# Kernel tuning notes

Hardware: AMD Instinct MI355X
Metric: run time of the kernel (lower is better)

The kernel has to match this reference:

```python
import jax, jax.numpy as jnp
import numpy as np

ALPHA_MAX = 0.1


def setup_inputs() -> dict:
    key = jax.random.key(0)
    ks = jax.random.split(key, 9)
    B, M, L = 256, 3, 100000
    A, H = 4096, 512
    return {
        "x": jax.random.uniform(ks[0], (B, M, L), dtype=jnp.float32),  # log1p scores, non-negative
        "active_idx": jax.random.randint(ks[1], (A,), 0, L, dtype=jnp.int64 if jax.config.jax_enable_x64 else jnp.int32),
        "global_logits": jnp.log(jnp.full((M,), 1.0 / M, dtype=jnp.float32) + 1e-12),
        "delta_w": 0.01 * jax.random.normal(ks[2], (M, L), dtype=jnp.float32),
        "bias": 0.01 * jax.random.normal(ks[3], (L,), dtype=jnp.float32),
        "log_alpha": jnp.float32(-3.0),
        "hidden_w": jax.random.normal(ks[4], (H, M * A), dtype=jnp.float32) * (1.0 / np.sqrt(M * A)),
        "hidden_b": 0.01 * jax.random.normal(ks[5], (H,), dtype=jnp.float32),
        "delta_layer_w": jax.random.normal(ks[6], (A, H), dtype=jnp.float32) * (1.0 / np.sqrt(H)),
        "delta_layer_b": 0.01 * jax.random.normal(ks[7], (A,), dtype=jnp.float32),
    }


def reference(x, active_idx, global_logits, delta_w, bias, log_alpha,
              hidden_w, hidden_b, delta_layer_w, delta_layer_b):
    B = x.shape[0]
    # base logits: elementwise weighted sum over the 3 models, per-label weights
    w_eff = jax.nn.softmax(global_logits)[:, None] + delta_w          # (M, L)
    logits = jnp.einsum("bml,ml->bl", x, w_eff) + bias                # (B, L)
    # gather active labels -> 2-layer MLP (dropout is identity in eval)
    x_active = x[:, :, active_idx].reshape(B, -1)                     # (B, M*A)
    h = jax.nn.relu(x_active @ hidden_w.T + hidden_b)                 # (B, H)
    delta_active = h @ delta_layer_w.T + delta_layer_b                # (B, A)
    # scaled scatter-add back into full logits (duplicates accumulate)
    alpha = ALPHA_MAX * jax.nn.sigmoid(log_alpha)
    logits = logits.at[:, active_idx].add(alpha * delta_active)
    return logits
```

## Files before the change

kernel.cpp:

```cpp
#include <hip/hip_runtime.h>
#include <math.h>

#define B_ 256
#define M_ 3
#define L_ 100000
#define A_ 4096
#define H_ 512
#define MA_ (M_*A_)
#define K1_ MA_
#define NZ_ 16
#define KC1_ (K1_/NZ_)
#define BCHUNK_ 4

#define NB_LG_   6272
#define NB_LGX_  98
#define NB_HW_   3072
#define NB_W2_   1024

typedef __attribute__((ext_vector_type(8))) short bf16x8;
typedef __attribute__((ext_vector_type(8))) unsigned short u16x8;
typedef __attribute__((ext_vector_type(4))) float f32x4;
typedef __attribute__((ext_vector_type(4))) int i32x4;

static __device__ __forceinline__ f32x4 ld4(const float* p) {
    return *reinterpret_cast<const f32x4*>(p);
}
static __device__ __forceinline__ f32x4 ld4nt(const float* p) {
    return __builtin_nontemporal_load(reinterpret_cast<const f32x4*>(p));
}
static __device__ __forceinline__ void st4nt(float* p, f32x4 v) {
    __builtin_nontemporal_store(v, reinterpret_cast<f32x4*>(p));
}
static __device__ __forceinline__ unsigned short f2bf(float f) {
    unsigned u = __float_as_uint(f);
    unsigned r = (u + 0x7FFFu + ((u >> 16) & 1u)) >> 16;
    return (unsigned short)r;
}

__global__ void init_head(int* __restrict__ head) {
    int i = blockIdx.x * blockDim.x + threadIdx.x;
    if (i < L_ / 4) {
        i32x4 m1 = {-1, -1, -1, -1};
        *reinterpret_cast<i32x4*>(head + i * 4) = m1;
    }
}

__global__ void build_head(const int* __restrict__ idx, int* __restrict__ head) {
    int a = blockIdx.x * blockDim.x + threadIdx.x;
    if (a < A_) head[idx[a]] = a;
}

__global__ __launch_bounds__(256) void mega(
    const float* __restrict__ x, const float* __restrict__ gl,
    const float* __restrict__ dw, const float* __restrict__ bias,
    const int* __restrict__ head,
    float* __restrict__ logits, unsigned short* __restrict__ xa,
    const float* __restrict__ hw, unsigned short* __restrict__ hwb,
    const float* __restrict__ w2, unsigned short* __restrict__ w2b) {
    int bid = blockIdx.x;
    int tid = threadIdx.x;

    if (bid >= NB_LG_) {
        const float* src;
        unsigned short* dst;
        int i;
        if (bid < NB_LG_ + NB_HW_) { src = hw; dst = hwb; i = (bid - NB_LG_) * 256 + tid; }
        else                       { src = w2; dst = w2b; i = (bid - NB_LG_ - NB_HW_) * 256 + tid; }
        f32x4 v0 = ld4nt(src + (size_t)i * 8);
        f32x4 v1 = ld4nt(src + (size_t)i * 8 + 4);
        u16x8 o;
        o[0] = f2bf(v0.x); o[1] = f2bf(v0.y); o[2] = f2bf(v0.z); o[3] = f2bf(v0.w);
        o[4] = f2bf(v1.x); o[5] = f2bf(v1.y); o[6] = f2bf(v1.z); o[7] = f2bf(v1.w);
        *reinterpret_cast<u16x8*>(dst + (size_t)i * 8) = o;
        return;
    }

    const int L4 = L_ / 4;
    int i = (bid % NB_LGX_) * 256 + tid;
    if (i >= L4) return;
    int l = i * 4;
    int b0 = (bid / NB_LGX_) * BCHUNK_;

    float g0 = gl[0], g1 = gl[1], g2 = gl[2];
    float mx = fmaxf(g0, fmaxf(g1, g2));
    float e0 = expf(g0 - mx), e1 = expf(g1 - mx), e2 = expf(g2 - mx);
    float inv = 1.0f / (e0 + e1 + e2);
    float s0 = e0 * inv, s1 = e1 * inv, s2 = e2 * inv;

    f32x4 d0 = ld4(dw + l);
    f32x4 d1 = ld4(dw + L_ + l);
    f32x4 d2 = ld4(dw + 2 * L_ + l);
    f32x4 bb = ld4(bias + l);
    f32x4 w0 = d0 + s0;
    f32x4 w1 = d1 + s1;
    f32x4 w2v = d2 + s2;

    i32x4 heads = *reinterpret_cast<const i32x4*>(head + l);

    f32x4 X[BCHUNK_][3];
    #pragma unroll
    for (int c = 0; c < BCHUNK_; ++c) {
        const float* xb = x + (size_t)(b0 + c) * M_ * L_ + l;
        X[c][0] = ld4nt(xb);
        X[c][1] = ld4nt(xb + L_);
        X[c][2] = ld4nt(xb + 2 * L_);
    }
    #pragma unroll
    for (int c = 0; c < BCHUNK_; ++c) {
        f32x4 o = X[c][0] * w0 + X[c][1] * w1 + X[c][2] * w2v + bb;
        st4nt(logits + (size_t)(b0 + c) * L_ + l, o);
    }

    #pragma unroll
    for (int c = 0; c < 4; ++c) {
        int a = heads[c];
        if (a >= 0) {
            #pragma unroll
            for (int b = 0; b < BCHUNK_; ++b) {
                unsigned short* xab = xa + (size_t)(b0 + b) * MA_;
                xab[a]          = f2bf(X[b][0][c]);
                xab[A_ + a]     = f2bf(X[b][1][c]);
                xab[2 * A_ + a] = f2bf(X[b][2][c]);
            }
        }
    }
}

__global__ void fixup(const int* __restrict__ idx, const int* __restrict__ head,
                      unsigned short* __restrict__ xa) {
    int t = blockIdx.x * blockDim.x + threadIdx.x;
    if (t >= B_ * A_) return;
    int a = t & (A_ - 1);
    int b = t >> 12;
    int ha = head[idx[a]];
    if (ha == a) return;
    unsigned short* xab = xa + (size_t)b * MA_;
    xab[a]          = xab[ha];
    xab[A_ + a]     = xab[A_ + ha];
    xab[2 * A_ + a] = xab[2 * A_ + ha];
}

__global__ __launch_bounds__(256) void gemm1_mfma(
    const unsigned short* __restrict__ Xa, const unsigned short* __restrict__ W,
    float* __restrict__ part) {
    int tid = threadIdx.x;
    int wave = tid >> 6, lane = tid & 63;
    int row0 = blockIdx.x * 64 + (wave >> 1) * 32;
    int col0 = blockIdx.y * 64 + (wave & 1) * 32;
    int k0 = blockIdx.z * KC1_;
    int lr = lane & 15;
    int lk = (lane >> 4) * 8;
    const unsigned short* pa0 = Xa + (size_t)(row0 + lr) * K1_ + k0 + lk;
    const unsigned short* pa1 = pa0 + (size_t)16 * K1_;
    const unsigned short* pb0 = W + (size_t)(col0 + lr) * K1_ + k0 + lk;
    const unsigned short* pb1 = pb0 + (size_t)16 * K1_;
    f32x4 acc00 = {0.f,0.f,0.f,0.f}, acc01 = {0.f,0.f,0.f,0.f};
    f32x4 acc10 = {0.f,0.f,0.f,0.f}, acc11 = {0.f,0.f,0.f,0.f};
    #pragma unroll 4
    for (int k = 0; k < KC1_; k += 32) {
        bf16x8 a0 = *reinterpret_cast<const bf16x8*>(pa0 + k);
        bf16x8 a1 = *reinterpret_cast<const bf16x8*>(pa1 + k);
        bf16x8 b0 = *reinterpret_cast<const bf16x8*>(pb0 + k);
        bf16x8 b1 = *reinterpret_cast<const bf16x8*>(pb1 + k);
        acc00 = __builtin_amdgcn_mfma_f32_16x16x32_bf16(a0, b0, acc00, 0, 0, 0);
        acc01 = __builtin_amdgcn_mfma_f32_16x16x32_bf16(a0, b1, acc01, 0, 0, 0);
        acc10 = __builtin_amdgcn_mfma_f32_16x16x32_bf16(a1, b0, acc10, 0, 0, 0);
        acc11 = __builtin_amdgcn_mfma_f32_16x16x32_bf16(a1, b1, acc11, 0, 0, 0);
    }
    float* base = part + (size_t)blockIdx.z * B_ * H_;
    #pragma unroll
    for (int j = 0; j < 4; ++j) {
        int r = (lane >> 4) * 4 + j;
        base[(size_t)(row0 + r) * H_ + col0 + lr]           = acc00[j];
        base[(size_t)(row0 + r) * H_ + col0 + 16 + lr]      = acc01[j];
        base[(size_t)(row0 + 16 + r) * H_ + col0 + lr]      = acc10[j];
        base[(size_t)(row0 + 16 + r) * H_ + col0 + 16 + lr] = acc11[j];
    }
}

__global__ void reduce_relu(const float* __restrict__ part,
                            const float* __restrict__ hb,
                            unsigned short* __restrict__ h) {
    int t = blockIdx.x * blockDim.x + threadIdx.x;
    if (t >= B_ * H_) return;
    int n = t & (H_ - 1);
    float s = hb[n];
    #pragma unroll
    for (int z = 0; z < NZ_; ++z) s += part[(size_t)z * B_ * H_ + t];
    h[t] = f2bf(fmaxf(s, 0.0f));
}

__global__ __launch_bounds__(256) void gemm2_scatter(
    const unsigned short* __restrict__ Hm, const unsigned short* __restrict__ W2,
    const float* __restrict__ b2, const float* __restrict__ la,
    const int* __restrict__ idx, float* __restrict__ logits) {
    int tid = threadIdx.x;
    int wave = tid >> 6, lane = tid & 63;
    int row0 = blockIdx.x * 64 + (wave >> 1) * 32;
    int col0 = blockIdx.y * 64 + (wave & 1) * 32;
    int lr = lane & 15;
    int lk = (lane >> 4) * 8;
    const unsigned short* pa0 = Hm + (size_t)(row0 + lr) * H_ + lk;
    const unsigned short* pa1 = pa0 + (size_t)16 * H_;
    const unsigned short* pb0 = W2 + (size_t)(col0 + lr) * H_ + lk;
    const unsigned short* pb1 = pb0 + (size_t)16 * H_;
    f32x4 acc00 = {0.f,0.f,0.f,0.f}, acc01 = {0.f,0.f,0.f,0.f};
    f32x4 acc10 = {0.f,0.f,0.f,0.f}, acc11 = {0.f,0.f,0.f,0.f};
    #pragma unroll 4
    for (int k = 0; k < H_; k += 32) {
        bf16x8 a0 = *reinterpret_cast<const bf16x8*>(pa0 + k);
        bf16x8 a1 = *reinterpret_cast<const bf16x8*>(pa1 + k);
        bf16x8 b0 = *reinterpret_cast<const bf16x8*>(pb0 + k);
        bf16x8 b1 = *reinterpret_cast<const bf16x8*>(pb1 + k);
        acc00 = __builtin_amdgcn_mfma_f32_16x16x32_bf16(a0, b0, acc00, 0, 0, 0);
        acc01 = __builtin_amdgcn_mfma_f32_16x16x32_bf16(a0, b1, acc01, 0, 0, 0);
        acc10 = __builtin_amdgcn_mfma_f32_16x16x32_bf16(a1, b0, acc10, 0, 0, 0);
        acc11 = __builtin_amdgcn_mfma_f32_16x16x32_bf16(a1, b1, acc11, 0, 0, 0);
    }
    float alpha = 0.1f / (1.0f + expf(-la[0]));
    int c0 = col0 + lr, c1 = col0 + 16 + lr;
    int l0 = idx[c0], l1 = idx[c1];
    float bias0 = b2[c0], bias1 = b2[c1];
    #pragma unroll
    for (int j = 0; j < 4; ++j) {
        int r = (lane >> 4) * 4 + j;
        atomicAdd(&logits[(size_t)(row0 + r) * L_ + l0],      alpha * (acc00[j] + bias0));
        atomicAdd(&logits[(size_t)(row0 + r) * L_ + l1],      alpha * (acc01[j] + bias1));
        atomicAdd(&logits[(size_t)(row0 + 16 + r) * L_ + l0], alpha * (acc10[j] + bias0));
        atomicAdd(&logits[(size_t)(row0 + 16 + r) * L_ + l1], alpha * (acc11[j] + bias1));
    }
}

static inline size_t align256(size_t x) { return (x + 255) & ~(size_t)255; }

extern "C" void kernel_launch(void* const* d_in, const int* in_sizes, int n_in,
                              void* d_out, int out_size, void* d_ws, size_t ws_size,
                              hipStream_t stream) {
    const float* x    = (const float*)d_in[0];
    const int*   idx  = (const int*)d_in[1];
    const float* gl   = (const float*)d_in[2];
    const float* dw   = (const float*)d_in[3];
    const float* bias = (const float*)d_in[4];
    const float* la   = (const float*)d_in[5];
    const float* hw   = (const float*)d_in[6];
    const float* hb   = (const float*)d_in[7];
    const float* w2   = (const float*)d_in[8];
    const float* b2   = (const float*)d_in[9];
    float* logits = (float*)d_out;

    char* ws = (char*)d_ws;
    int* head = (int*)ws;                      ws += align256((size_t)L_ * 4);
    unsigned short* xa = (unsigned short*)ws;  ws += align256((size_t)B_ * MA_ * 2);
    unsigned short* hwb = (unsigned short*)ws; ws += align256((size_t)H_ * MA_ * 2);
    unsigned short* w2b = (unsigned short*)ws; ws += align256((size_t)A_ * H_ * 2);
    float* part = (float*)ws;                  ws += align256((size_t)NZ_ * B_ * H_ * 4);
    unsigned short* h = (unsigned short*)ws;   ws += align256((size_t)B_ * H_ * 2);

    init_head<<<(L_ / 4 + 255) / 256, 256, 0, stream>>>(head);
    build_head<<<(A_ + 255) / 256, 256, 0, stream>>>(idx, head);

    mega<<<NB_LG_ + NB_HW_ + NB_W2_, 256, 0, stream>>>(
        x, gl, dw, bias, head, logits, xa, hw, hwb, w2, w2b);

    fixup<<<(B_ * A_ + 255) / 256, 256, 0, stream>>>(idx, head, xa);

    gemm1_mfma<<<dim3(B_ / 64, H_ / 64, NZ_), 256, 0, stream>>>(xa, hwb, part);
    reduce_relu<<<(B_ * H_ + 255) / 256, 256, 0, stream>>>(part, hb, h);
    gemm2_scatter<<<dim3(B_ / 64, A_ / 64), 256, 0, stream>>>(h, w2b, b2, la, idx, logits);
}
```

Baseline: 202.3 us.

## Sort active labels into positional order so xa writes are local; drop fixup pass

Builds a permutation of the active indices sorted by label position, using a per-window histogram and rank-based placement. The gathered activation matrix xa is then written in sorted column order, and duplicate labels are written directly, so the separate fixup kernel is removed. The K dimension of the hidden weight is permuted to match while it is cast to bf16. The point is to make the scattered xa writes contiguous per window and save one launch, at the cost of two small setup kernels and gathered reads of hidden_w during the conversion.

```diff
diff --git a/kernel.cpp b/kernel.cpp
--- a/kernel.cpp
+++ b/kernel.cpp
@@ -12,8 +12,9 @@
 #define KC1_ (K1_/NZ_)
 #define BCHUNK_ 4
 
-#define NB_LG_   6272
+#define NWIN_    98
 #define NB_LGX_  98
+#define NB_LG_   (NB_LGX_*(B_/BCHUNK_))
 #define NB_HW_   3072
 #define NB_W2_   1024
 
@@ -45,15 +46,56 @@
     }
 }
 
-__global__ void build_head(const int* __restrict__ idx, int* __restrict__ head) {
-    int a = blockIdx.x * blockDim.x + threadIdx.x;
-    if (a < A_) head[idx[a]] = a;
+__global__ void window_hist(const int* __restrict__ idx, int* __restrict__ jbase) {
+    __shared__ int cnt[NWIN_];
+    for (int w = threadIdx.x; w < NWIN_; w += 256) cnt[w] = 0;
+    __syncthreads();
+    for (int a = threadIdx.x; a < A_; a += 256) atomicAdd(&cnt[idx[a] >> 10], 1);
+    __syncthreads();
+    if (threadIdx.x == 0) {
+        int s = 0;
+        for (int w = 0; w < NWIN_; ++w) { jbase[w] = s; s += cnt[w]; }
+        jbase[NWIN_] = s;
+    }
+}
+
+__global__ void build_perm(const int* __restrict__ idx, const int* __restrict__ jbase,
+                           int* __restrict__ a_of_j, int* __restrict__ l_of_j,
+                           int* __restrict__ head2) {
+    __shared__ int ml[A_];
+    __shared__ int ma[A_];
+    __shared__ int nm_sh;
+    int w = blockIdx.x, tid = threadIdx.x;
+    if (tid == 0) nm_sh = 0;
+    __syncthreads();
+    for (int a = tid; a < A_; a += 256) {
+        int l = idx[a];
+        if ((l >> 10) == w) { int p = atomicAdd(&nm_sh, 1); ml[p] = l; ma[p] = a; }
+    }
+    __syncthreads();
+    int nm = nm_sh;
+    int base = jbase[w];
+    for (int p = tid; p < nm; p += 256) {
+        int l = ml[p], a = ma[p];
+        int rank = 0, same_smaller = 0;
+        for (int q = 0; q < nm; ++q) {
+            int lq = ml[q], aq = ma[q];
+            rank += (lq < l) | ((lq == l) & (aq < a));
+            same_smaller += ((lq == l) & (aq < a));
+        }
+        int j = base + rank;
+        a_of_j[j] = a;
+        l_of_j[j] = l;
+        if (same_smaller == 0) head2[l] = j;
+    }
+    if (w == 0 && tid == 0) l_of_j[A_] = -1;
 }
 
 __global__ __launch_bounds__(256) void mega(
     const float* __restrict__ x, const float* __restrict__ gl,
     const float* __restrict__ dw, const float* __restrict__ bias,
-    const int* __restrict__ head,
+    const int* __restrict__ head2, const int* __restrict__ l_of_j,
+    const int* __restrict__ a_of_j,
     float* __restrict__ logits, unsigned short* __restrict__ xa,
     const float* __restrict__ hw, unsigned short* __restrict__ hwb,
     const float* __restrict__ w2, unsigned short* __restrict__ w2b) {
@@ -61,17 +103,26 @@
     int tid = threadIdx.x;
 
     if (bid >= NB_LG_) {
-        const float* src;
-        unsigned short* dst;
-        int i;
-        if (bid < NB_LG_ + NB_HW_) { src = hw; dst = hwb; i = (bid - NB_LG_) * 256 + tid; }
-        else                       { src = w2; dst = w2b; i = (bid - NB_LG_ - NB_HW_) * 256 + tid; }
-        f32x4 v0 = ld4nt(src + (size_t)i * 8);
-        f32x4 v1 = ld4nt(src + (size_t)i * 8 + 4);
-        u16x8 o;
-        o[0] = f2bf(v0.x); o[1] = f2bf(v0.y); o[2] = f2bf(v0.z); o[3] = f2bf(v0.w);
-        o[4] = f2bf(v1.x); o[5] = f2bf(v1.y); o[6] = f2bf(v1.z); o[7] = f2bf(v1.w);
-        *reinterpret_cast<u16x8*>(dst + (size_t)i * 8) = o;
+        if (bid < NB_LG_ + NB_HW_) {
+            int i = (bid - NB_LG_) * 256 + tid;
+            int o = i * 8;
+            int n = o / MA_;
+            int col = o % MA_;
+            int m = col >> 12, j0 = col & (A_ - 1);
+            const float* row = hw + (size_t)n * MA_ + (m << 12);
+            u16x8 out;
+            #pragma unroll
+            for (int t = 0; t < 8; ++t) out[t] = f2bf(row[a_of_j[j0 + t]]);
+            *reinterpret_cast<u16x8*>(hwb + (size_t)o) = out;
+        } else {
+            int i = (bid - NB_LG_ - NB_HW_) * 256 + tid;
+            f32x4 v0 = ld4nt(w2 + (size_t)i * 8);
+            f32x4 v1 = ld4nt(w2 + (size_t)i * 8 + 4);
+            u16x8 o;
+            o[0] = f2bf(v0.x); o[1] = f2bf(v0.y); o[2] = f2bf(v0.z); o[3] = f2bf(v0.w);
+            o[4] = f2bf(v1.x); o[5] = f2bf(v1.y); o[6] = f2bf(v1.z); o[7] = f2bf(v1.w);
+            *reinterpret_cast<u16x8*>(w2b + (size_t)i * 8) = o;
+        }
         return;
     }
 
@@ -87,15 +138,12 @@
     float inv = 1.0f / (e0 + e1 + e2);
     float s0 = e0 * inv, s1 = e1 * inv, s2 = e2 * inv;
 
-    f32x4 d0 = ld4(dw + l);
-    f32x4 d1 = ld4(dw + L_ + l);
-    f32x4 d2 = ld4(dw + 2 * L_ + l);
+    f32x4 w0 = ld4(dw + l) + s0;
+    f32x4 w1 = ld4(dw + L_ + l) + s1;
+    f32x4 w2v = ld4(dw + 2 * L_ + l) + s2;
     f32x4 bb = ld4(bias + l);
-    f32x4 w0 = d0 + s0;
-    f32x4 w1 = d1 + s1;
-    f32x4 w2v = d2 + s2;
-
-    i32x4 heads = *reinterpret_cast<const i32x4*>(head + l);
+
+    i32x4 heads = *reinterpret_cast<const i32x4*>(head2 + l);
 
     f32x4 X[BCHUNK_][3];
     #pragma unroll
@@ -113,31 +161,21 @@
 
     #pragma unroll
     for (int c = 0; c < 4; ++c) {
-        int a = heads[c];
-        if (a >= 0) {
-            #pragma unroll
-            for (int b = 0; b < BCHUNK_; ++b) {
-                unsigned short* xab = xa + (size_t)(b0 + b) * MA_;
-                xab[a]          = f2bf(X[b][0][c]);
-                xab[A_ + a]     = f2bf(X[b][1][c]);
-                xab[2 * A_ + a] = f2bf(X[b][2][c]);
-            }
+        int j = heads[c];
+        if (j >= 0) {
+            int lh = l + c;
+            do {
+                #pragma unroll
+                for (int b = 0; b < BCHUNK_; ++b) {
+                    unsigned short* xab = xa + (size_t)(b0 + b) * MA_;
+                    xab[j]          = f2bf(X[b][0][c]);
+                    xab[A_ + j]     = f2bf(X[b][1][c]);
+                    xab[2 * A_ + j] = f2bf(X[b][2][c]);
+                }
+                ++j;
+            } while (l_of_j[j] == lh);
         }
     }
-}
-
-__global__ void fixup(const int* __restrict__ idx, const int* __restrict__ head,
-                      unsigned short* __restrict__ xa) {
-    int t = blockIdx.x * blockDim.x + threadIdx.x;
-    if (t >= B_ * A_) return;
-    int a = t & (A_ - 1);
-    int b = t >> 12;
-    int ha = head[idx[a]];
-    if (ha == a) return;
-    unsigned short* xab = xa + (size_t)b * MA_;
-    xab[a]          = xab[ha];
-    xab[A_ + a]     = xab[A_ + ha];
-    xab[2 * A_ + a] = xab[2 * A_ + ha];
 }
 
 __global__ __launch_bounds__(256) void gemm1_mfma(
@@ -249,20 +287,22 @@
     float* logits = (float*)d_out;
 
     char* ws = (char*)d_ws;
-    int* head = (int*)ws;                      ws += align256((size_t)L_ * 4);
+    int* head2 = (int*)ws;                     ws += align256((size_t)L_ * 4);
+    int* jbase = (int*)ws;                     ws += align256((size_t)(NWIN_ + 1) * 4);
+    int* a_of_j = (int*)ws;                    ws += align256((size_t)A_ * 4);
+    int* l_of_j = (int*)ws;                    ws += align256((size_t)(A_ + 1) * 4);
     unsigned short* xa = (unsigned short*)ws;  ws += align256((size_t)B_ * MA_ * 2);
     unsigned short* hwb = (unsigned short*)ws; ws += align256((size_t)H_ * MA_ * 2);
     unsigned short* w2b = (unsigned short*)ws; ws += align256((size_t)A_ * H_ * 2);
     float* part = (float*)ws;                  ws += align256((size_t)NZ_ * B_ * H_ * 4);
     unsigned short* h = (unsigned short*)ws;   ws += align256((size_t)B_ * H_ * 2);
 
-    init_head<<<(L_ / 4 + 255) / 256, 256, 0, stream>>>(head);
-    build_head<<<(A_ + 255) / 256, 256, 0, stream>>>(idx, head);
+    init_head<<<(L_ / 4 + 255) / 256, 256, 0, stream>>>(head2);
+    window_hist<<<1, 256, 0, stream>>>(idx, jbase);
+    build_perm<<<NWIN_, 256, 0, stream>>>(idx, jbase, a_of_j, l_of_j, head2);
 
     mega<<<NB_LG_ + NB_HW_ + NB_W2_, 256, 0, stream>>>(
-        x, gl, dw, bias, head, logits, xa, hw, hwb, w2, w2b);
-
-    fixup<<<(B_ * A_ + 255) / 256, 256, 0, stream>>>(idx, head, xa);
+        x, gl, dw, bias, head2, l_of_j, a_of_j, logits, xa, hw, hwb, w2, w2b);
 
     gemm1_mfma<<<dim3(B_ / 64, H_ / 64, NZ_), 256, 0, stream>>>(xa, hwb, part);
     reduce_relu<<<(B_ * H_ + 255) / 256, 256, 0, stream>>>(part, hb, h);
```

New measurement: 199.3 us. Within noise of the previous version (-1.5%).
